# Optimization experiments

Measured on AMD Instinct MI355X. Metric: run time of the kernel, lower is better.

## Reference

```python
import jax, jax.numpy as jnp
import numpy as np

N = 8192

def _gcn_layer(x, src, dst, W, b, norm_out, norm_in, activation=None):
    # DGL GraphConv, norm='both': D_in^{-1/2} A D_out^{-1/2} X W + b
    xw = x @ W                              # [N, out] (weight first: in>=out)
    m = (xw * norm_out[:, None])[src]       # gather per-edge messages [E, out]
    agg = jax.ops.segment_sum(m, dst, num_segments=N)
    h = agg * norm_in[:, None] + b
    return activation(h) if activation is not None else h


def setup_inputs() -> dict:
    key = jax.random.key(0)
    k1, k2, k3, k4, k5 = jax.random.split(key, 5)
    E = 262144
    in_dim, h1, h2 = 512, 256, 64
    features = jax.random.normal(k1, (N, in_dim), dtype=jnp.float32)
    src = jax.random.randint(k2, (E,), 0, N)
    dst = jax.random.randint(k3, (E,), 0, N)
    W1 = jax.random.normal(k4, (in_dim, h1), dtype=jnp.float32) / np.sqrt(in_dim)
    b1 = jnp.zeros((h1,), dtype=jnp.float32)
    W2 = jax.random.normal(k5, (h1, h2), dtype=jnp.float32) / np.sqrt(h1)
    b2 = jnp.zeros((h2,), dtype=jnp.float32)
    return {"features": features, "src": src, "dst": dst,
            "W1": W1, "b1": b1, "W2": W2, "b2": b2}


def reference(features, src, dst, W1, b1, W2, b2):
    # Degrees and symmetric normalization (clamp(min=1) as in DGL GraphConv).
    ones = jnp.ones(src.shape[0], dtype=features.dtype)
    deg_out = jax.ops.segment_sum(ones, src, num_segments=N)
    deg_in = jax.ops.segment_sum(ones, dst, num_segments=N)
    norm_out = jnp.maximum(deg_out, 1.0) ** -0.5
    norm_in = jnp.maximum(deg_in, 1.0) ** -0.5
    # Encoder (dropout is identity in eval mode).
    h = _gcn_layer(features, src, dst, W1, b1, norm_out, norm_in, jax.nn.relu)
    z = _gcn_layer(h, src, dst, W2, b2, norm_out, norm_in, None)
    # Dot-product decoder.
    adj_rec = jax.nn.sigmoid(z @ z.T)       # [N, N]
    return adj_rec
```

## Files before the change

### kernel.cpp

```cpp
#include <hip/hip_runtime.h>
#include <hip/hip_bf16.h>
#include <math.h>

#define NNODES 8192
#define NEDGES 262144
#define INDIM  512
#define H1     256
#define H2     64

typedef __attribute__((ext_vector_type(8))) short bf16x8;
typedef __attribute__((ext_vector_type(4))) float f32x4;

static __device__ __forceinline__ float bf2f(unsigned short u) {
    return __uint_as_float((unsigned)u << 16);
}
static __device__ __forceinline__ unsigned short f2bf(float f) {
    __hip_bfloat16 h = __float2bfloat16(f);
    return *(unsigned short*)&h;
}


__global__ void prepdeg_kernel(const float* __restrict__ features, __hip_bfloat16* __restrict__ featb,
                               const float* __restrict__ W1, __hip_bfloat16* __restrict__ w1t,
                               const float* __restrict__ W2, __hip_bfloat16* __restrict__ w2t,
                               const int* __restrict__ src, const int* __restrict__ dst,
                               int* deg_out, int* deg_in) {
    int b = blockIdx.x;
    if (b < 4096) {
        int t = b * 256 + threadIdx.x;
        float4 v = ((const float4*)features)[t];
        ushort4 o;
        o.x = f2bf(v.x); o.y = f2bf(v.y); o.z = f2bf(v.z); o.w = f2bf(v.w);
        ((ushort4*)featb)[t] = o;
    } else if (b < 4608) {
        int t = (b - 4096) * 256 + threadIdx.x;
        int k = t / H1, c = t % H1;
        w1t[(size_t)c * INDIM + k] = __float2bfloat16(W1[t]);
    } else if (b < 4672) {
        int t = (b - 4608) * 256 + threadIdx.x;
        int k = t / H2, c = t % H2;
        w2t[(size_t)c * H1 + k] = __float2bfloat16(W2[t]);
    } else {
        int e = (b - 4672) * 256 + threadIdx.x;
        atomicAdd(&deg_out[src[e]], 1);
        atomicAdd(&deg_in[dst[e]], 1);
    }
}


__global__ __launch_bounds__(1024) void scannorm_kernel(const int* __restrict__ deg_in,
                                                        const int* __restrict__ deg_out,
                                                        int* __restrict__ row_start,
                                                        float* __restrict__ norm_out,
                                                        float* __restrict__ norm_in) {
    __shared__ int part[1024];
    int t = threadIdx.x;
    int v[8]; int s = 0;
#pragma unroll
    for (int u = 0; u < 8; u++) { v[u] = deg_in[t * 8 + u]; s += v[u]; }
    part[t] = s; __syncthreads();
    for (int off = 1; off < 1024; off <<= 1) {
        int x = part[t];
        if (t >= off) x += part[t - off];
        __syncthreads();
        part[t] = x;
        __syncthreads();
    }
    int run = part[t] - s;
#pragma unroll
    for (int u = 0; u < 8; u++) {
        int n = t * 8 + u;
        row_start[n] = run; run += v[u];
        norm_in[n]  = 1.0f / sqrtf(fmaxf((float)v[u], 1.0f));
        norm_out[n] = 1.0f / sqrtf(fmaxf((float)deg_out[n], 1.0f));
    }
    if (t == 1023) row_start[NNODES] = run;
}


template<int K, int MT, int NT, int NOUT>
__device__ __forceinline__ void gemm_tile(const short* __restrict__ A, const short* __restrict__ BT,
                                          const float* __restrict__ scale, short* __restrict__ out,
                                          int bx, int by, int tid) {
    constexpr int AM = MT / 64;
    constexpr int BN = NT / 16;
    const int lane = tid & 63;
    const int wid  = tid >> 6;
    const int i0 = by * MT + wid * (MT / 4);
    const int j0 = bx * NT;
    const int fr = lane & 15;
    const int kg = lane >> 4;

    f32x4 acc[AM][BN] = {};
    for (int k0 = 0; k0 < K; k0 += 32) {
        bf16x8 a[AM], b[BN];
#pragma unroll
        for (int m = 0; m < AM; m++)
            a[m] = *(const bf16x8*)&A[(size_t)(i0 + m * 16 + fr) * K + k0 + kg * 8];
#pragma unroll
        for (int n = 0; n < BN; n++)
            b[n] = *(const bf16x8*)&BT[(size_t)(j0 + n * 16 + fr) * K + k0 + kg * 8];
#pragma unroll
        for (int m = 0; m < AM; m++)
#pragma unroll
            for (int n = 0; n < BN; n++)
                acc[m][n] = __builtin_amdgcn_mfma_f32_16x16x32_bf16(a[m], b[n], acc[m][n], 0, 0, 0);
    }

    const int col = lane & 15;
    const int rg4 = (lane >> 4) * 4;
#pragma unroll
    for (int m = 0; m < AM; m++)
#pragma unroll
        for (int r = 0; r < 4; r++) {
            int row = i0 + m * 16 + rg4 + r;
            float sc = scale[row];
#pragma unroll
            for (int n = 0; n < BN; n++)
                out[(size_t)row * NOUT + j0 + n * 16 + col] = f2bf(acc[m][n][r] * sc);
        }
}


__global__ __launch_bounds__(256) void bucketgemm_kernel(const int* __restrict__ src, const int* __restrict__ dst,
                                                         const int* __restrict__ row_start, int* cursor,
                                                         int* __restrict__ sorted_src,
                                                         const __hip_bfloat16* __restrict__ featb,
                                                         const __hip_bfloat16* __restrict__ w1t,
                                                         const float* __restrict__ norm_out,
                                                         __hip_bfloat16* __restrict__ xwb) {
    int b = blockIdx.x;
    if (b < 1024) {
        int e = b * 256 + threadIdx.x;
        int d = dst[e];
        int p = atomicAdd(&cursor[d], 1);
        sorted_src[row_start[d] + p] = src[e];
    } else {
        int g = b - 1024;
        gemm_tile<INDIM, 64, 64, H1>((const short*)featb, (const short*)w1t, norm_out,
                                     (short*)xwb, g & 3, g >> 2, threadIdx.x);
    }
}


__global__ __launch_bounds__(1024) void agg_gemm2_kernel(const int* __restrict__ row_start,
                                                         const int* __restrict__ sorted_src,
                                                         const __hip_bfloat16* __restrict__ msgb,
                                                         const float* __restrict__ norm_in,
                                                         const float* __restrict__ norm_out,
                                                         const float* __restrict__ b1,
                                                         const __hip_bfloat16* __restrict__ w2t,
                                                         __hip_bfloat16* __restrict__ hwb) {
    __shared__ short hs[16][H1 + 8];
    const ushort4* msg = (const ushort4*)msgb;
    const int wid  = threadIdx.x >> 6;
    const int lane = threadIdx.x & 63;
    const int n0 = blockIdx.x * 16;
    {
        int n = n0 + wid;
        int e0 = row_start[n], e1 = row_start[n + 1];
        float ax = 0.f, ay = 0.f, az = 0.f, aw = 0.f;
        int e = e0;
        for (; e + 1 < e1; e += 2) {
            int s0 = sorted_src[e], s1 = sorted_src[e + 1];
            ushort4 v0 = msg[(size_t)s0 * 64 + lane];
            ushort4 v1 = msg[(size_t)s1 * 64 + lane];
            ax += bf2f(v0.x) + bf2f(v1.x);
            ay += bf2f(v0.y) + bf2f(v1.y);
            az += bf2f(v0.z) + bf2f(v1.z);
            aw += bf2f(v0.w) + bf2f(v1.w);
        }
        if (e < e1) {
            ushort4 v0 = msg[(size_t)sorted_src[e] * 64 + lane];
            ax += bf2f(v0.x); ay += bf2f(v0.y); az += bf2f(v0.z); aw += bf2f(v0.w);
        }
        float ni = norm_in[n];
        float4 bb = ((const float4*)b1)[lane];
        ushort4 o;
        o.x = f2bf(fmaxf(ax * ni + bb.x, 0.f));
        o.y = f2bf(fmaxf(ay * ni + bb.y, 0.f));
        o.z = f2bf(fmaxf(az * ni + bb.z, 0.f));
        o.w = f2bf(fmaxf(aw * ni + bb.w, 0.f));
        *(ushort4*)&hs[wid][lane * 4] = o;
    }
    __syncthreads();
    if (wid < 4) {
        const short* BT = (const short*)w2t;
        const int fr = lane & 15;
        const int kg = lane >> 4;
        const int j0 = wid * 16;
        f32x4 acc = {};
#pragma unroll
        for (int k0 = 0; k0 < H1; k0 += 32) {
            bf16x8 a = *(const bf16x8*)&hs[fr][k0 + kg * 8];
            bf16x8 b = *(const bf16x8*)&BT[(size_t)(j0 + fr) * H1 + k0 + kg * 8];
            acc = __builtin_amdgcn_mfma_f32_16x16x32_bf16(a, b, acc, 0, 0, 0);
        }
        const int col = lane & 15;
        const int rg4 = (lane >> 4) * 4;
#pragma unroll
        for (int r = 0; r < 4; r++) {
            int nn = n0 + rg4 + r;
            hwb[(size_t)nn * H2 + j0 + col] = __float2bfloat16(acc[r] * norm_out[nn]);
        }
    }
}


__global__ void agg64_kernel(const int* __restrict__ row_start, const int* __restrict__ sorted_src,
                             const __hip_bfloat16* __restrict__ msgb, const float* __restrict__ norm_in,
                             const float* __restrict__ bias, __hip_bfloat16* __restrict__ outb) {
    const unsigned* msg = (const unsigned*)msgb;
    int n = blockIdx.x;
    int lane = threadIdx.x;
    int half = lane >> 5, li = lane & 31;
    int e0 = row_start[n], e1 = row_start[n + 1];
    float ax = 0.f, ay = 0.f;
    for (int e = e0 + half; e < e1; e += 2) {
        unsigned u = msg[(size_t)sorted_src[e] * 32 + li];
        ax += bf2f((unsigned short)(u & 0xffff));
        ay += bf2f((unsigned short)(u >> 16));
    }
    ax += __shfl_xor(ax, 32);
    ay += __shfl_xor(ay, 32);
    if (half == 0) {
        float ni = norm_in[n];
        float z0 = ax * ni + bias[2 * li];
        float z1 = ay * ni + bias[2 * li + 1];
        unsigned o = (unsigned)f2bf(z0) | ((unsigned)f2bf(z1) << 16);
        ((unsigned*)outb)[(size_t)n * 32 + li] = o;
    }
}


#define LSTR 132

__global__ __launch_bounds__(256) void decoder_mfma_kernel(const __hip_bfloat16* __restrict__ zbf,
                                                           float* __restrict__ out) {
    __shared__ float lds[4][16 * LSTR];
    const short* zb = (const short*)zbf;
    const int lane = threadIdx.x & 63;
    const int wid  = threadIdx.x >> 6;
    const int i0 = blockIdx.y * 128 + wid * 32;
    const int j0 = blockIdx.x * 128;
    const int fr = lane & 15;
    const int kg = lane >> 4;

    f32x4 acc[2][8] = {};
#pragma unroll
    for (int ks = 0; ks < 2; ks++) {
        bf16x8 a[2], b[8];
#pragma unroll
        for (int m = 0; m < 2; m++)
            a[m] = *(const bf16x8*)&zb[(size_t)(i0 + m * 16 + fr) * H2 + ks * 32 + kg * 8];
#pragma unroll
        for (int n = 0; n < 8; n++)
            b[n] = *(const bf16x8*)&zb[(size_t)(j0 + n * 16 + fr) * H2 + ks * 32 + kg * 8];
#pragma unroll
        for (int m = 0; m < 2; m++)
#pragma unroll
            for (int n = 0; n < 8; n++)
                acc[m][n] = __builtin_amdgcn_mfma_f32_16x16x32_bf16(a[m], b[n], acc[m][n], 0, 0, 0);
    }

    float mx = 0.f;
#pragma unroll
    for (int m = 0; m < 2; m++)
#pragma unroll
        for (int n = 0; n < 8; n++)
#pragma unroll
            for (int r = 0; r < 4; r++)
                mx = fmaxf(mx, fabsf(acc[m][n][r]));
    const bool useExp = __any(mx > 1.0f);

    const int col = lane & 15;
    const int rg4 = (lane >> 4) * 4;
    float* L = lds[wid];
    const int rrow = (lane >> 5);
    const int rcol = (lane & 31) * 4;

#pragma unroll
    for (int m = 0; m < 2; m++) {
#pragma unroll
        for (int n = 0; n < 8; n++)
#pragma unroll
            for (int r = 0; r < 4; r++) {
                float x = acc[m][n][r];
                float s;
                if (useExp) {
                    s = 1.f / (1.f + __expf(-x));
                } else {
                    float u = x * x;
                    s = 0.5f + x * (0.25f + u * (-0.0208333333f + u * 0.0020833333f));
                }
                L[(rg4 + r) * LSTR + n * 16 + col] = s;
            }
#pragma unroll
        for (int i = 0; i < 8; i++) {
            int row = i * 2 + rrow;
            float4 v = *(float4*)&L[row * LSTR + rcol];
            *(float4*)&out[(size_t)(i0 + m * 16 + row) * NNODES + j0 + rcol] = v;
        }
    }
}


extern "C" void kernel_launch(void* const* d_in, const int* in_sizes, int n_in,
                              void* d_out, int out_size, void* d_ws, size_t ws_size,
                              hipStream_t stream) {
    const float* features = (const float*)d_in[0];
    const int*   src      = (const int*)d_in[1];
    const int*   dst      = (const int*)d_in[2];
    const float* W1       = (const float*)d_in[3];
    const float* b1       = (const float*)d_in[4];
    const float* W2       = (const float*)d_in[5];
    const float* b2       = (const float*)d_in[6];
    float* out = (float*)d_out;

    char* p = (char*)d_ws;
    auto alloc = [&](size_t bytes) -> void* {
        void* q = (void*)p;
        p += (bytes + 255) & ~(size_t)255;
        return q;
    };
    int*   deg_out_i  = (int*)alloc(NNODES * 4);
    int*   deg_in_i   = (int*)alloc(NNODES * 4);
    int*   cursor     = (int*)alloc(NNODES * 4);
    int*   row_start  = (int*)alloc((NNODES + 1) * 4);
    float* norm_out   = (float*)alloc(NNODES * 4);
    float* norm_in    = (float*)alloc(NNODES * 4);
    int*   sorted_src = (int*)alloc(NEDGES * 4);
    __hip_bfloat16* featb = (__hip_bfloat16*)alloc((size_t)NNODES * INDIM * 2);
    __hip_bfloat16* w1t   = (__hip_bfloat16*)alloc((size_t)H1 * INDIM * 2);
    __hip_bfloat16* w2t   = (__hip_bfloat16*)alloc((size_t)H2 * H1 * 2);
    __hip_bfloat16* xwb   = (__hip_bfloat16*)alloc((size_t)NNODES * H1 * 2);
    __hip_bfloat16* hwb   = (__hip_bfloat16*)alloc((size_t)NNODES * H2 * 2);
    __hip_bfloat16* zb    = (__hip_bfloat16*)alloc((size_t)NNODES * H2 * 2);

    hipMemsetAsync(deg_out_i, 0, 3 * NNODES * 4, stream);
    prepdeg_kernel<<<4672 + NEDGES / 256, 256, 0, stream>>>(
        features, featb, W1, w1t, W2, w2t, src, dst, deg_out_i, deg_in_i);
    scannorm_kernel<<<1, 1024, 0, stream>>>(deg_in_i, deg_out_i,
                                            row_start, norm_out, norm_in);
    bucketgemm_kernel<<<1024 + 512, 256, 0, stream>>>(
        src, dst, row_start, cursor, sorted_src, featb, w1t, norm_out, xwb);
    agg_gemm2_kernel<<<NNODES / 16, 1024, 0, stream>>>(
        row_start, sorted_src, xwb, norm_in, norm_out, b1, w2t, hwb);
    agg64_kernel<<<NNODES, 64, 0, stream>>>(row_start, sorted_src, hwb,
                                            norm_in, b2, zb);
    decoder_mfma_kernel<<<dim3(NNODES / 128, NNODES / 128), 256, 0, stream>>>(
        zb, out);
}
```

Measured before the change: 181.3 us.

## Replace 16-node MFMA agg+GEMM2 block with per-node wavefront scalar GEMV

The layer-1 aggregation and second GEMM move from 1024-thread blocks covering 16 nodes (with MFMA for the 16x256x64 product) to one 64-thread block per node. Each lane aggregates its slice, writes h in fp32 to LDS, then computes one output column as a scalar dot product over W2 kept in row-major bf16. The aim is to shed the block-wide barrier and idle waves during the small MFMA stage and to add parallelism and finer load balance across nodes. In exchange, every block rereads all of W2 (32 KB, likely cache-resident) and the MFMA is replaced by 256 scalar FMAs per lane.

```diff
diff --git a/kernel.cpp b/kernel.cpp
--- a/kernel.cpp
+++ b/kernel.cpp
@@ -7,6 +7,7 @@
 #define INDIM  512
 #define H1     256
 #define H2     64
+#define LSTR   132
 
 typedef __attribute__((ext_vector_type(8))) short bf16x8;
 typedef __attribute__((ext_vector_type(4))) float f32x4;
@@ -22,7 +23,7 @@
 
 __global__ void prepdeg_kernel(const float* __restrict__ features, __hip_bfloat16* __restrict__ featb,
                                const float* __restrict__ W1, __hip_bfloat16* __restrict__ w1t,
-                               const float* __restrict__ W2, __hip_bfloat16* __restrict__ w2t,
+                               const float* __restrict__ W2, __hip_bfloat16* __restrict__ w2b,
                                const int* __restrict__ src, const int* __restrict__ dst,
                                int* deg_out, int* deg_in) {
     int b = blockIdx.x;
@@ -38,8 +39,7 @@
         w1t[(size_t)c * INDIM + k] = __float2bfloat16(W1[t]);
     } else if (b < 4672) {
         int t = (b - 4608) * 256 + threadIdx.x;
-        int k = t / H2, c = t % H2;
-        w2t[(size_t)c * H1 + k] = __float2bfloat16(W2[t]);
+        w2b[t] = __float2bfloat16(W2[t]);
     } else {
         int e = (b - 4672) * 256 + threadIdx.x;
         atomicAdd(&deg_out[src[e]], 1);
@@ -143,67 +143,52 @@
 }
 
 
-__global__ __launch_bounds__(1024) void agg_gemm2_kernel(const int* __restrict__ row_start,
-                                                         const int* __restrict__ sorted_src,
-                                                         const __hip_bfloat16* __restrict__ msgb,
-                                                         const float* __restrict__ norm_in,
-                                                         const float* __restrict__ norm_out,
-                                                         const float* __restrict__ b1,
-                                                         const __hip_bfloat16* __restrict__ w2t,
-                                                         __hip_bfloat16* __restrict__ hwb) {
-    __shared__ short hs[16][H1 + 8];
+__global__ void aggfused_kernel(const int* __restrict__ row_start, const int* __restrict__ sorted_src,
+                                const __hip_bfloat16* __restrict__ msgb,
+                                const float* __restrict__ norm_in, const float* __restrict__ norm_out,
+                                const float* __restrict__ b1, const __hip_bfloat16* __restrict__ w2b,
+                                __hip_bfloat16* __restrict__ hwb) {
+    __shared__ float hs[H1];
     const ushort4* msg = (const ushort4*)msgb;
-    const int wid  = threadIdx.x >> 6;
-    const int lane = threadIdx.x & 63;
-    const int n0 = blockIdx.x * 16;
-    {
-        int n = n0 + wid;
-        int e0 = row_start[n], e1 = row_start[n + 1];
-        float ax = 0.f, ay = 0.f, az = 0.f, aw = 0.f;
-        int e = e0;
-        for (; e + 1 < e1; e += 2) {
-            int s0 = sorted_src[e], s1 = sorted_src[e + 1];
-            ushort4 v0 = msg[(size_t)s0 * 64 + lane];
-            ushort4 v1 = msg[(size_t)s1 * 64 + lane];
-            ax += bf2f(v0.x) + bf2f(v1.x);
-            ay += bf2f(v0.y) + bf2f(v1.y);
-            az += bf2f(v0.z) + bf2f(v1.z);
-            aw += bf2f(v0.w) + bf2f(v1.w);
-        }
-        if (e < e1) {
-            ushort4 v0 = msg[(size_t)sorted_src[e] * 64 + lane];
-            ax += bf2f(v0.x); ay += bf2f(v0.y); az += bf2f(v0.z); aw += bf2f(v0.w);
-        }
-        float ni = norm_in[n];
-        float4 bb = ((const float4*)b1)[lane];
-        ushort4 o;
-        o.x = f2bf(fmaxf(ax * ni + bb.x, 0.f));
-        o.y = f2bf(fmaxf(ay * ni + bb.y, 0.f));
-        o.z = f2bf(fmaxf(az * ni + bb.z, 0.f));
-        o.w = f2bf(fmaxf(aw * ni + bb.w, 0.f));
-        *(ushort4*)&hs[wid][lane * 4] = o;
-    }
+    const unsigned short* w2 = (const unsigned short*)w2b;
+    int n = blockIdx.x;
+    int lane = threadIdx.x;
+    int e0 = row_start[n], e1 = row_start[n + 1];
+    float ax = 0.f, ay = 0.f, az = 0.f, aw = 0.f;
+    int e = e0;
+    for (; e + 1 < e1; e += 2) {
+        int s0 = sorted_src[e], s1 = sorted_src[e + 1];
+        ushort4 v0 = msg[(size_t)s0 * 64 + lane];
+        ushort4 v1 = msg[(size_t)s1 * 64 + lane];
+        ax += bf2f(v0.x) + bf2f(v1.x);
+        ay += bf2f(v0.y) + bf2f(v1.y);
+        az += bf2f(v0.z) + bf2f(v1.z);
+        aw += bf2f(v0.w) + bf2f(v1.w);
+    }
+    if (e < e1) {
+        ushort4 v0 = msg[(size_t)sorted_src[e] * 64 + lane];
+        ax += bf2f(v0.x); ay += bf2f(v0.y); az += bf2f(v0.z); aw += bf2f(v0.w);
+    }
+    float ni = norm_in[n];
+    float4 bb = ((const float4*)b1)[lane];
+    float4 h;
+    h.x = fmaxf(ax * ni + bb.x, 0.f);
+    h.y = fmaxf(ay * ni + bb.y, 0.f);
+    h.z = fmaxf(az * ni + bb.z, 0.f);
+    h.w = fmaxf(aw * ni + bb.w, 0.f);
+    *(float4*)&hs[lane * 4] = h;
     __syncthreads();
-    if (wid < 4) {
-        const short* BT = (const short*)w2t;
-        const int fr = lane & 15;
-        const int kg = lane >> 4;
-        const int j0 = wid * 16;
-        f32x4 acc = {};
-#pragma unroll
-        for (int k0 = 0; k0 < H1; k0 += 32) {
-            bf16x8 a = *(const bf16x8*)&hs[fr][k0 + kg * 8];
-            bf16x8 b = *(const bf16x8*)&BT[(size_t)(j0 + fr) * H1 + k0 + kg * 8];
-            acc = __builtin_amdgcn_mfma_f32_16x16x32_bf16(a, b, acc, 0, 0, 0);
-        }
-        const int col = lane & 15;
-        const int rg4 = (lane >> 4) * 4;
-#pragma unroll
-        for (int r = 0; r < 4; r++) {
-            int nn = n0 + rg4 + r;
-            hwb[(size_t)nn * H2 + j0 + col] = __float2bfloat16(acc[r] * norm_out[nn]);
-        }
-    }
+
+    float acc = 0.f;
+#pragma unroll 8
+    for (int k0 = 0; k0 < H1; k0 += 4) {
+        float4 hv = *(const float4*)&hs[k0];
+        acc += hv.x * bf2f(w2[(k0 + 0) * H2 + lane])
+             + hv.y * bf2f(w2[(k0 + 1) * H2 + lane])
+             + hv.z * bf2f(w2[(k0 + 2) * H2 + lane])
+             + hv.w * bf2f(w2[(k0 + 3) * H2 + lane]);
+    }
+    hwb[(size_t)n * H2 + lane] = __float2bfloat16(acc * norm_out[n]);
 }
 
 
@@ -233,8 +218,6 @@
 }
 
 
-#define LSTR 132
-
 __global__ __launch_bounds__(256) void decoder_mfma_kernel(const __hip_bfloat16* __restrict__ zbf,
                                                            float* __restrict__ out) {
     __shared__ float lds[4][16 * LSTR];
@@ -276,7 +259,7 @@
     const int col = lane & 15;
     const int rg4 = (lane >> 4) * 4;
     float* L = lds[wid];
-    const int rrow = (lane >> 5);
+    const int rrow = lane >> 5;
     const int rcol = (lane & 31) * 4;
 
 #pragma unroll
@@ -332,20 +315,20 @@
     int*   sorted_src = (int*)alloc(NEDGES * 4);
     __hip_bfloat16* featb = (__hip_bfloat16*)alloc((size_t)NNODES * INDIM * 2);
     __hip_bfloat16* w1t   = (__hip_bfloat16*)alloc((size_t)H1 * INDIM * 2);
-    __hip_bfloat16* w2t   = (__hip_bfloat16*)alloc((size_t)H2 * H1 * 2);
+    __hip_bfloat16* w2b   = (__hip_bfloat16*)alloc((size_t)H1 * H2 * 2);
     __hip_bfloat16* xwb   = (__hip_bfloat16*)alloc((size_t)NNODES * H1 * 2);
     __hip_bfloat16* hwb   = (__hip_bfloat16*)alloc((size_t)NNODES * H2 * 2);
     __hip_bfloat16* zb    = (__hip_bfloat16*)alloc((size_t)NNODES * H2 * 2);
 
     hipMemsetAsync(deg_out_i, 0, 3 * NNODES * 4, stream);
     prepdeg_kernel<<<4672 + NEDGES / 256, 256, 0, stream>>>(
-        features, featb, W1, w1t, W2, w2t, src, dst, deg_out_i, deg_in_i);
+        features, featb, W1, w1t, W2, w2b, src, dst, deg_out_i, deg_in_i);
     scannorm_kernel<<<1, 1024, 0, stream>>>(deg_in_i, deg_out_i,
                                             row_start, norm_out, norm_in);
     bucketgemm_kernel<<<1024 + 512, 256, 0, stream>>>(
         src, dst, row_start, cursor, sorted_src, featb, w1t, norm_out, xwb);
-    agg_gemm2_kernel<<<NNODES / 16, 1024, 0, stream>>>(
-        row_start, sorted_src, xwb, norm_in, norm_out, b1, w2t, hwb);
+    aggfused_kernel<<<NNODES, 64, 0, stream>>>(
+        row_start, sorted_src, xwb, norm_in, norm_out, b1, w2b, hwb);
     agg64_kernel<<<NNODES, 64, 0, stream>>>(row_start, sorted_src, hwb,
                                             norm_in, b2, zb);
     decoder_mfma_kernel<<<dim3(NNODES / 128, NNODES / 128), 256, 0, stream>>>(
```

After: 185.9 us. 1.03x slower.
